# Kernel tuning notes

Measured on AMD Instinct MI355X. Metric: run time of the kernel, lower is better.

Reference implementation:

```python
import jax, jax.numpy as jnp
import numpy as np

N_NODES = 100000
N_EDGES = 1600000
HIDDEN = 128
BN_EPS = 1e-5


def setup_inputs() -> dict:
    key = jax.random.key(0)
    ks = jax.random.split(key, 6)
    x0 = jax.random.normal(ks[0], (N_NODES, HIDDEN), dtype=jnp.float32)
    x1 = jax.random.normal(ks[1], (N_NODES, HIDDEN), dtype=jnp.float32)
    edge_index = jax.random.randint(ks[2], (2, N_EDGES), 0, N_NODES, dtype=jnp.int64)
    mean_weight = jnp.ones((2,), dtype=jnp.float32)
    # GIN MLP: Linear(h,h) -> ReLU -> Linear(h,h); scale ~ torch default init
    scale = 1.0 / np.sqrt(HIDDEN)
    W1 = jax.random.normal(ks[3], (HIDDEN, HIDDEN), dtype=jnp.float32) * scale
    b1 = jnp.zeros((HIDDEN,), dtype=jnp.float32)
    W2 = jax.random.normal(ks[4], (HIDDEN, HIDDEN), dtype=jnp.float32) * scale
    b2 = jnp.zeros((HIDDEN,), dtype=jnp.float32)
    gamma = jnp.ones((HIDDEN,), dtype=jnp.float32)
    beta = jnp.zeros((HIDDEN,), dtype=jnp.float32)
    return {"x0": x0, "x1": x1, "edge_index": edge_index,
            "mean_weight": mean_weight, "W1": W1, "b1": b1,
            "W2": W2, "b2": b2, "gamma": gamma, "beta": beta}


def reference(x0, x1, edge_index, mean_weight, W1, b1, W2, b2, gamma, beta):
    # sigmoid-gated sum of the two node-feature inputs (no drop-path: deterministic eval)
    s = jax.nn.sigmoid(mean_weight)
    out = s[0] * x0 + s[1] * x1                      # [N, H]
    # GINConv, eps=0: h = MLP(x + sum_{j in N(i)} x_j)
    src, dst = edge_index[0], edge_index[1]
    agg = jax.ops.segment_sum(out[src], dst, num_segments=out.shape[0])  # scatter-add [N, H]
    h = out + agg
    h = jnp.maximum(h @ W1 + b1, 0.0) @ W2 + b2      # Linear-ReLU-Linear
    # BatchNorm1d, training-mode batch statistics (biased variance)
    mean = jnp.mean(h, axis=0)
    var = jnp.var(h, axis=0)
    hn = (h - mean) * jax.lax.rsqrt(var + BN_EPS)
    return hn * gamma + beta
```

## Files before the change

### kernel.cpp

```cpp
#include <hip/hip_runtime.h>
#include <math.h>

#define N_NODES 100000
#define N_EDGES 1600000
#define HID 128
#define BN_EPS 1e-5f
#define BM 64
#define NTILES ((N_NODES + BM - 1) / BM)
#define MLP_BLOCKS 512
#define NSUB 16
#define NPW 4

typedef __attribute__((ext_vector_type(8))) short bf16x8;
typedef __attribute__((ext_vector_type(4))) float f32x4;

__device__ inline unsigned short f2bf(float f) {
    unsigned u = __float_as_uint(f);
    unsigned r = u + 0x7FFFu + ((u >> 16) & 1u);
    return (unsigned short)(r >> 16);
}
__device__ inline unsigned pk2(float lo, float hi) {
    return (unsigned)f2bf(lo) | ((unsigned)f2bf(hi) << 16);
}
__device__ inline float bflo(unsigned u) { return __uint_as_float(u << 16); }
__device__ inline float bfhi(unsigned u) { return __uint_as_float(u & 0xffff0000u); }

__global__ __launch_bounds__(256) void k_gate(const float* __restrict__ x0,
                                              const float* __restrict__ x1,
                                              const float* __restrict__ mw,
                                              unsigned* __restrict__ gate_u2,
                                              float* __restrict__ shadow,
                                              int* __restrict__ head,
                                              const float* __restrict__ W1,
                                              const float* __restrict__ W2,
                                              unsigned short* __restrict__ W1T,
                                              unsigned short* __restrict__ W2T) {
    int t = blockIdx.x * 256 + threadIdx.x;
    if (blockIdx.x < 64) shadow[t] = 0.0f;
    if (t < NSUB * N_NODES) head[t] = -1;
    if (t < HID * HID) {
        int k = t >> 7, n = t & 127;
        W1T[n * HID + k] = f2bf(W1[t]);
        W2T[n * HID + k] = f2bf(W2[t]);
    }
    float s0 = 1.0f / (1.0f + expf(-mw[0]));
    float s1 = 1.0f / (1.0f + expf(-mw[1]));
    float4 a = ((const float4*)x0)[t];
    float4 b = ((const float4*)x1)[t];
    uint2 o;
    o.x = pk2(s0 * a.x + s1 * b.x, s0 * a.y + s1 * b.y);
    o.y = pk2(s0 * a.z + s1 * b.z, s0 * a.w + s1 * b.w);
    ((uint2*)gate_u2)[t] = o;
}

__global__ __launch_bounds__(256) void k_build(const int* __restrict__ ei,
                                               int* __restrict__ head,
                                               int2* __restrict__ pair) {
    int e = blockIdx.x * 256 + threadIdx.x;
    int src = ei[e];
    int dst = ei[N_EDGES + e];
    int old = atomicExch(&head[(e & (NSUB - 1)) * N_NODES + dst], e);
    pair[e] = make_int2(src, old);
}

__global__ __launch_bounds__(256) void k_agg(const unsigned* __restrict__ gu,
                                             const int2* __restrict__ pair,
                                             const int* __restrict__ head,
                                             unsigned* __restrict__ hbuf_u) {
    int wid = threadIdx.x >> 6, lane = threadIdx.x & 63;
    int nbase = (blockIdx.x * 4 + wid) * NPW;
    int e = head[(lane & 15) * N_NODES + (nbase + (lane >> 4))];

    float sx[NPW], sy[NPW];
#pragma unroll
    for (int j = 0; j < NPW; ++j) {
        unsigned g = gu[(size_t)(nbase + j) * 64 + lane];
        sx[j] = bflo(g); sy[j] = bfhi(g);
    }

    while (__any(e >= 0)) {
        int2 pv = make_int2(-1, -1);
        if (e >= 0) pv = pair[e];
#pragma unroll
        for (int j = 0; j < 64; ++j) {
            int sv = __builtin_amdgcn_readlane(pv.x, j);
            if (sv >= 0) {
                unsigned v = gu[(size_t)sv * 64 + lane];
                sx[j >> 4] += bflo(v);
                sy[j >> 4] += bfhi(v);
            }
        }
        e = pv.y;
    }
#pragma unroll
    for (int j = 0; j < NPW; ++j)
        hbuf_u[(size_t)(nbase + j) * 64 + lane] = pk2(sx[j], sy[j]);
}

__global__ __launch_bounds__(256, 2) void k_mlp(unsigned short* __restrict__ hbuf,
                                                const unsigned short* __restrict__ W1T,
                                                const unsigned short* __restrict__ W2T,
                                                const float* __restrict__ b1,
                                                const float* __restrict__ b2,
                                                float* __restrict__ shadow) {
    __shared__ short lds_x[BM * HID];
    __shared__ short lds_w1[HID * HID];
    __shared__ short lds_w2[HID * HID];

    const int tid = threadIdx.x;

    for (int c = tid; c < 2048; c += 256) {
        int n = c >> 4, k16 = c & 15;
        int4 v1 = ((const int4*)W1T)[c];
        int4 v2 = ((const int4*)W2T)[c];
        int boff = n * 256 + ((k16 * 16) ^ ((n & 7) << 4));
        *(int4*)((char*)lds_w1 + boff) = v1;
        *(int4*)((char*)lds_w2 + boff) = v2;
    }

    const int wid = tid >> 6, lane = tid & 63;
    const int wrow = wid >> 1, wcol = wid & 1;
    const int l15 = lane & 15, l4 = lane >> 4;

    float b1g[4], b2g[4];
#pragma unroll
    for (int nf = 0; nf < 4; ++nf) {
        int n = wcol * 64 + nf * 16 + l15;
        b1g[nf] = b1[n];
        b2g[nf] = b2[n];
    }

    float psum[4] = {0.f, 0.f, 0.f, 0.f}, psq[4] = {0.f, 0.f, 0.f, 0.f};

    __syncthreads();

    for (int tile = blockIdx.x; tile < NTILES; tile += MLP_BLOCKS) {
        const int m0 = tile * BM;

        for (int c = tid; c < BM * 16; c += 256) {
            int r = c >> 4, k16 = c & 15;
            int row = m0 + r;
            int4 v = {0, 0, 0, 0};
            if (row < N_NODES)
                v = ((const int4*)(hbuf + (size_t)row * HID))[k16];
            int boff = r * 256 + ((k16 * 16) ^ ((r & 7) << 4));
            *(int4*)((char*)lds_x + boff) = v;
        }
        __syncthreads();

        f32x4 acc1[2][4];
#pragma unroll
        for (int mf = 0; mf < 2; ++mf)
#pragma unroll
            for (int nf = 0; nf < 4; ++nf) acc1[mf][nf] = (f32x4){0.f, 0.f, 0.f, 0.f};

#pragma unroll
        for (int kc = 0; kc < 4; ++kc) {
            bf16x8 av[2], bv[4];
#pragma unroll
            for (int mf = 0; mf < 2; ++mf) {
                int r = wrow * 32 + mf * 16 + l15;
                int boff = r * 256 + (((kc * 64) + l4 * 16) ^ ((r & 7) << 4));
                av[mf] = *(const bf16x8*)((const char*)lds_x + boff);
            }
#pragma unroll
            for (int nf = 0; nf < 4; ++nf) {
                int n = wcol * 64 + nf * 16 + l15;
                int boff = n * 256 + (((kc * 64) + l4 * 16) ^ ((n & 7) << 4));
                bv[nf] = *(const bf16x8*)((const char*)lds_w1 + boff);
            }
#pragma unroll
            for (int mf = 0; mf < 2; ++mf)
#pragma unroll
                for (int nf = 0; nf < 4; ++nf)
                    acc1[mf][nf] = __builtin_amdgcn_mfma_f32_16x16x32_bf16(av[mf], bv[nf], acc1[mf][nf], 0, 0, 0);
        }

        __syncthreads();

#pragma unroll
        for (int mf = 0; mf < 2; ++mf)
#pragma unroll
            for (int nf = 0; nf < 4; ++nf) {
                int n = wcol * 64 + nf * 16 + l15;
#pragma unroll
                for (int r = 0; r < 4; ++r) {
                    int row = wrow * 32 + mf * 16 + l4 * 4 + r;
                    float v = fmaxf(acc1[mf][nf][r] + b1g[nf], 0.f);
                    int boff = row * 256 + ((2 * n) ^ ((row & 7) << 4));
                    *(unsigned short*)((char*)lds_x + boff) = f2bf(v);
                }
            }

        __syncthreads();

        f32x4 acc2[2][4];
#pragma unroll
        for (int mf = 0; mf < 2; ++mf)
#pragma unroll
            for (int nf = 0; nf < 4; ++nf) acc2[mf][nf] = (f32x4){0.f, 0.f, 0.f, 0.f};

#pragma unroll
        for (int kc = 0; kc < 4; ++kc) {
            bf16x8 av[2], bv[4];
#pragma unroll
            for (int mf = 0; mf < 2; ++mf) {
                int r = wrow * 32 + mf * 16 + l15;
                int boff = r * 256 + (((kc * 64) + l4 * 16) ^ ((r & 7) << 4));
                av[mf] = *(const bf16x8*)((const char*)lds_x + boff);
            }
#pragma unroll
            for (int nf = 0; nf < 4; ++nf) {
                int n = wcol * 64 + nf * 16 + l15;
                int boff = n * 256 + (((kc * 64) + l4 * 16) ^ ((n & 7) << 4));
                bv[nf] = *(const bf16x8*)((const char*)lds_w2 + boff);
            }
#pragma unroll
            for (int mf = 0; mf < 2; ++mf)
#pragma unroll
                for (int nf = 0; nf < 4; ++nf)
                    acc2[mf][nf] = __builtin_amdgcn_mfma_f32_16x16x32_bf16(av[mf], bv[nf], acc2[mf][nf], 0, 0, 0);
        }

#pragma unroll
        for (int mf = 0; mf < 2; ++mf)
#pragma unroll
            for (int nf = 0; nf < 4; ++nf) {
                int n = wcol * 64 + nf * 16 + l15;
#pragma unroll
                for (int r = 0; r < 4; ++r) {
                    int row = m0 + wrow * 32 + mf * 16 + l4 * 4 + r;
                    float v = acc2[mf][nf][r] + b2g[nf];
                    if (row < N_NODES) {
                        unsigned short q = f2bf(v);
                        float vq = __uint_as_float(((unsigned)q) << 16);
                        hbuf[(size_t)row * HID + n] = q;
                        psum[nf] += vq;
                        psq[nf] += vq * vq;
                    }
                }
            }

        __syncthreads();
    }

    float* cs = (float*)lds_x;
    cs[tid] = 0.f;
    __syncthreads();
#pragma unroll
    for (int nf = 0; nf < 4; ++nf) {
        float s = psum[nf], q = psq[nf];
        s += __shfl_xor(s, 16); q += __shfl_xor(q, 16);
        s += __shfl_xor(s, 32); q += __shfl_xor(q, 32);
        if (lane < 16) {
            int n = wcol * 64 + nf * 16 + lane;
            atomicAdd(&cs[n], s);
            atomicAdd(&cs[HID + n], q);
        }
    }
    __syncthreads();
    atomicAdd(&shadow[(blockIdx.x & 63) * 256 + tid], cs[tid]);
}

__global__ void k_finalize(const float* __restrict__ shadow,
                           const float* __restrict__ gamma,
                           const float* __restrict__ beta,
                           float* __restrict__ sc) {
    int c = threadIdx.x;
    float sum = 0.f, sq = 0.f;
    for (int i = 0; i < 64; ++i) {
        sum += shadow[i * 256 + c];
        sq  += shadow[i * 256 + 128 + c];
    }
    float mean = sum * (1.0f / N_NODES);
    float var  = sq * (1.0f / N_NODES) - mean * mean;
    float r = rsqrtf(var + BN_EPS);
    float scale = gamma[c] * r;
    sc[c]       = scale;
    sc[128 + c] = beta[c] - mean * scale;
}

__global__ __launch_bounds__(256) void k_bn(const unsigned short* __restrict__ h2,
                                            const float* __restrict__ sc,
                                            float* __restrict__ out) {
    int t = blockIdx.x * 256 + threadIdx.x;
    int c4 = t & 31;
    float4 scale = ((const float4*)sc)[c4];
    float4 shift = ((const float4*)sc)[32 + c4];
    uint2 hv = ((const uint2*)h2)[t];
    float4 o;
    o.x = bflo(hv.x) * scale.x + shift.x;
    o.y = bfhi(hv.x) * scale.y + shift.y;
    o.z = bflo(hv.y) * scale.z + shift.z;
    o.w = bfhi(hv.y) * scale.w + shift.w;
    ((float4*)out)[t] = o;
}

extern "C" void kernel_launch(void* const* d_in, const int* in_sizes, int n_in,
                              void* d_out, int out_size, void* d_ws, size_t ws_size,
                              hipStream_t stream) {
    const float* x0 = (const float*)d_in[0];
    const float* x1 = (const float*)d_in[1];
    const int*   ei = (const int*)d_in[2];
    const float* mw = (const float*)d_in[3];
    const float* W1 = (const float*)d_in[4];
    const float* b1 = (const float*)d_in[5];
    const float* W2 = (const float*)d_in[6];
    const float* b2 = (const float*)d_in[7];
    const float* gamma = (const float*)d_in[8];
    const float* beta  = (const float*)d_in[9];

    float* out = (float*)d_out;

    unsigned short* hbuf = (unsigned short*)d_ws;
    float* shadow = (float*)(hbuf + (size_t)N_NODES * HID);
    float* sc     = shadow + 16384;
    unsigned short* W1T = (unsigned short*)(sc + 256);
    unsigned short* W2T = W1T + 16384;
    int* head    = (int*)(W2T + 16384);
    int2* pair   = (int2*)(head + NSUB * N_NODES);

    int nthread4 = N_NODES * HID / 4;

    k_gate<<<nthread4 / 256, 256, 0, stream>>>(x0, x1, mw, (unsigned*)out, shadow, head,
                                               W1, W2, W1T, W2T);
    k_build<<<N_EDGES / 256, 256, 0, stream>>>(ei, head, pair);
    k_agg<<<N_NODES / (4 * NPW), 256, 0, stream>>>((const unsigned*)out, pair, head,
                                                   (unsigned*)hbuf);
    k_mlp<<<MLP_BLOCKS, 256, 0, stream>>>(hbuf, W1T, W2T, b1, b2, shadow);
    k_finalize<<<1, 128, 0, stream>>>(shadow, gamma, beta, sc);
    k_bn<<<nthread4 / 256, 256, 0, stream>>>(hbuf, sc, out);
}
```

Baseline: 253.1 us.

## Fuse gate and edge-list build kernels; fold BN finalize into grid-stride BN kernel

Merges the gating/bf16 conversion kernel and the linked-list edge build kernel into one launch whose blocks are interleaved by role (two gate blocks per edge block). The head-array initialisation moves to a hipMemsetAsync so the atomicExch build no longer depends on a prior kernel. The separate BN finalize kernel is folded into the BN apply kernel: every block recomputes scale and shift from the shadow sums into shared memory, then processes elements with a grid-stride loop. This removes two launches and their serialization gaps, at the cost of redundant per-block finalize work.

```diff
diff --git a/kernel.cpp b/kernel.cpp
--- a/kernel.cpp
+++ b/kernel.cpp
@@ -10,6 +10,7 @@
 #define MLP_BLOCKS 512
 #define NSUB 16
 #define NPW 4
+#define BN_BLOCKS 512
 
 typedef __attribute__((ext_vector_type(8))) short bf16x8;
 typedef __attribute__((ext_vector_type(4))) float f32x4;
@@ -25,42 +26,44 @@
 __device__ inline float bflo(unsigned u) { return __uint_as_float(u << 16); }
 __device__ inline float bfhi(unsigned u) { return __uint_as_float(u & 0xffff0000u); }
 
-__global__ __launch_bounds__(256) void k_gate(const float* __restrict__ x0,
-                                              const float* __restrict__ x1,
-                                              const float* __restrict__ mw,
-                                              unsigned* __restrict__ gate_u2,
-                                              float* __restrict__ shadow,
-                                              int* __restrict__ head,
-                                              const float* __restrict__ W1,
-                                              const float* __restrict__ W2,
-                                              unsigned short* __restrict__ W1T,
-                                              unsigned short* __restrict__ W2T) {
-    int t = blockIdx.x * 256 + threadIdx.x;
-    if (blockIdx.x < 64) shadow[t] = 0.0f;
-    if (t < NSUB * N_NODES) head[t] = -1;
-    if (t < HID * HID) {
-        int k = t >> 7, n = t & 127;
-        W1T[n * HID + k] = f2bf(W1[t]);
-        W2T[n * HID + k] = f2bf(W2[t]);
-    }
-    float s0 = 1.0f / (1.0f + expf(-mw[0]));
-    float s1 = 1.0f / (1.0f + expf(-mw[1]));
-    float4 a = ((const float4*)x0)[t];
-    float4 b = ((const float4*)x1)[t];
-    uint2 o;
-    o.x = pk2(s0 * a.x + s1 * b.x, s0 * a.y + s1 * b.y);
-    o.y = pk2(s0 * a.z + s1 * b.z, s0 * a.w + s1 * b.w);
-    ((uint2*)gate_u2)[t] = o;
-}
-
-__global__ __launch_bounds__(256) void k_build(const int* __restrict__ ei,
+__global__ __launch_bounds__(256) void k_front(const float* __restrict__ x0,
+                                               const float* __restrict__ x1,
+                                               const float* __restrict__ mw,
+                                               unsigned* __restrict__ gate_u2,
+                                               float* __restrict__ shadow,
+                                               const float* __restrict__ W1,
+                                               const float* __restrict__ W2,
+                                               unsigned short* __restrict__ W1T,
+                                               unsigned short* __restrict__ W2T,
+                                               const int* __restrict__ ei,
                                                int* __restrict__ head,
                                                int2* __restrict__ pair) {
-    int e = blockIdx.x * 256 + threadIdx.x;
-    int src = ei[e];
-    int dst = ei[N_EDGES + e];
-    int old = atomicExch(&head[(e & (NSUB - 1)) * N_NODES + dst], e);
-    pair[e] = make_int2(src, old);
+    int bid = blockIdx.x, tid = threadIdx.x;
+    int role = bid % 3;
+    if (role < 2) {
+        int gid = (bid / 3) * 2 + role;
+        int t = gid * 256 + tid;
+        if (gid < 64) {
+            shadow[t] = 0.0f;
+            int k = t >> 7, n = t & 127;
+            W1T[n * HID + k] = f2bf(W1[t]);
+            W2T[n * HID + k] = f2bf(W2[t]);
+        }
+        float s0 = 1.0f / (1.0f + expf(-mw[0]));
+        float s1 = 1.0f / (1.0f + expf(-mw[1]));
+        float4 a = ((const float4*)x0)[t];
+        float4 b = ((const float4*)x1)[t];
+        uint2 o;
+        o.x = pk2(s0 * a.x + s1 * b.x, s0 * a.y + s1 * b.y);
+        o.y = pk2(s0 * a.z + s1 * b.z, s0 * a.w + s1 * b.w);
+        ((uint2*)gate_u2)[t] = o;
+    } else {
+        int e = (bid / 3) * 256 + tid;
+        int src = ei[e];
+        int dst = ei[N_EDGES + e];
+        int old = atomicExch(&head[(e & (NSUB - 1)) * N_NODES + dst], e);
+        pair[e] = make_int2(src, old);
+    }
 }
 
 __global__ __launch_bounds__(256) void k_agg(const unsigned* __restrict__ gu,
@@ -262,38 +265,40 @@
     atomicAdd(&shadow[(blockIdx.x & 63) * 256 + tid], cs[tid]);
 }
 
-__global__ void k_finalize(const float* __restrict__ shadow,
-                           const float* __restrict__ gamma,
-                           const float* __restrict__ beta,
-                           float* __restrict__ sc) {
-    int c = threadIdx.x;
-    float sum = 0.f, sq = 0.f;
-    for (int i = 0; i < 64; ++i) {
-        sum += shadow[i * 256 + c];
-        sq  += shadow[i * 256 + 128 + c];
-    }
-    float mean = sum * (1.0f / N_NODES);
-    float var  = sq * (1.0f / N_NODES) - mean * mean;
-    float r = rsqrtf(var + BN_EPS);
-    float scale = gamma[c] * r;
-    sc[c]       = scale;
-    sc[128 + c] = beta[c] - mean * scale;
-}
-
-__global__ __launch_bounds__(256) void k_bn(const unsigned short* __restrict__ h2,
-                                            const float* __restrict__ sc,
-                                            float* __restrict__ out) {
-    int t = blockIdx.x * 256 + threadIdx.x;
-    int c4 = t & 31;
+__global__ __launch_bounds__(256) void k_bn2(const unsigned short* __restrict__ h2,
+                                             const float* __restrict__ shadow,
+                                             const float* __restrict__ gamma,
+                                             const float* __restrict__ beta,
+                                             float* __restrict__ out) {
+    __shared__ float sc[256];
+    int tid = threadIdx.x;
+    if (tid < 128) {
+        float sum = 0.f, sq = 0.f;
+        for (int i = 0; i < 64; ++i) {
+            sum += shadow[i * 256 + tid];
+            sq  += shadow[i * 256 + 128 + tid];
+        }
+        float mean = sum * (1.0f / N_NODES);
+        float var  = sq * (1.0f / N_NODES) - mean * mean;
+        float r = rsqrtf(var + BN_EPS);
+        float scale = gamma[tid] * r;
+        sc[tid]       = scale;
+        sc[128 + tid] = beta[tid] - mean * scale;
+    }
+    __syncthreads();
+    int c4 = tid & 31;
     float4 scale = ((const float4*)sc)[c4];
     float4 shift = ((const float4*)sc)[32 + c4];
-    uint2 hv = ((const uint2*)h2)[t];
-    float4 o;
-    o.x = bflo(hv.x) * scale.x + shift.x;
-    o.y = bfhi(hv.x) * scale.y + shift.y;
-    o.z = bflo(hv.y) * scale.z + shift.z;
-    o.w = bfhi(hv.y) * scale.w + shift.w;
-    ((float4*)out)[t] = o;
+    const int total = N_NODES * HID / 4;
+    for (int t = blockIdx.x * 256 + tid; t < total; t += BN_BLOCKS * 256) {
+        uint2 hv = ((const uint2*)h2)[t];
+        float4 o;
+        o.x = bflo(hv.x) * scale.x + shift.x;
+        o.y = bfhi(hv.x) * scale.y + shift.y;
+        o.z = bflo(hv.y) * scale.z + shift.z;
+        o.w = bfhi(hv.y) * scale.w + shift.w;
+        ((float4*)out)[t] = o;
+    }
 }
 
 extern "C" void kernel_launch(void* const* d_in, const int* in_sizes, int n_in,
@@ -320,14 +325,12 @@
     int* head    = (int*)(W2T + 16384);
     int2* pair   = (int2*)(head + NSUB * N_NODES);
 
-    int nthread4 = N_NODES * HID / 4;
-
-    k_gate<<<nthread4 / 256, 256, 0, stream>>>(x0, x1, mw, (unsigned*)out, shadow, head,
-                                               W1, W2, W1T, W2T);
-    k_build<<<N_EDGES / 256, 256, 0, stream>>>(ei, head, pair);
+    hipMemsetAsync(head, 0xFF, (size_t)NSUB * N_NODES * sizeof(int), stream);
+
+    k_front<<<18750, 256, 0, stream>>>(x0, x1, mw, (unsigned*)out, shadow,
+                                       W1, W2, W1T, W2T, ei, head, pair);
     k_agg<<<N_NODES / (4 * NPW), 256, 0, stream>>>((const unsigned*)out, pair, head,
                                                    (unsigned*)hbuf);
     k_mlp<<<MLP_BLOCKS, 256, 0, stream>>>(hbuf, W1T, W2T, b1, b2, shadow);
-    k_finalize<<<1, 128, 0, stream>>>(shadow, gamma, beta, sc);
-    k_bn<<<nthread4 / 256, 256, 0, stream>>>(hbuf, sc, out);
-}
+    k_bn2<<<BN_BLOCKS, 256, 0, stream>>>(hbuf, shadow, gamma, beta, out);
+}
```

After: 242.1 us. 1.05x faster.
